# Kernel optimization log

Measured on AMD Instinct MI355X. Metric: run time of the kernel, lower is better.

## Reference

```python
import jax, jax.numpy as jnp
import numpy as np

N = 100000   # nodes
DEG = 16     # in-degree per node
E = N * DEG  # edges
D = 64       # embedding_dim


def mobius_addition(x, y, c):
    xy = jnp.sum(x * y, axis=-1, keepdims=True)
    x2 = jnp.sum(x * x, axis=-1, keepdims=True)
    y2 = jnp.sum(y * y, axis=-1, keepdims=True)
    num = (1 + 2 * c * xy + c * y2) * x + (1 - c * x2) * y
    den = 1 + 2 * c * xy + c * c * x2 * y2
    return num / den


def exp_map(x, v, c):
    vn = jnp.linalg.norm(v, axis=-1, keepdims=True)
    sc = jnp.sqrt(c)
    second = jnp.tanh(sc * vn / 2) * v / (sc * vn)
    return mobius_addition(x, second, c)


def log_map(x, y, c):
    add = mobius_addition(-x, y, c)
    an = jnp.linalg.norm(add, axis=-1, keepdims=True)
    sc = jnp.sqrt(c)
    return 2 / sc * jnp.arctanh(sc * an) * add / an


def setup_inputs() -> dict:
    key = jax.random.key(0)
    ks = jax.random.split(key, 6)
    # scale so points are well inside the Poincare ball (atanh domain)
    x = jax.random.normal(ks[0], (N, D), jnp.float32) * 0.01
    src = jax.random.randint(ks[1], (E,), 0, N, dtype=jnp.int32)
    # every node gets exactly DEG in-edges -> no isolated nodes (avoids 0/0 in exp_map)
    dst = jnp.repeat(jnp.arange(N, dtype=jnp.int32), DEG)
    s = 1.0 / np.sqrt(D)
    Wq = jax.random.normal(ks[2], (D, D), jnp.float32) * s
    Wk = jax.random.normal(ks[3], (D, D), jnp.float32) * s
    Wv = jax.random.normal(ks[4], (D, D), jnp.float32) * s
    bq = jnp.zeros((D,), jnp.float32)
    bk = jnp.zeros((D,), jnp.float32)
    bv = jnp.zeros((D,), jnp.float32)
    curvature = jnp.ones((1,), jnp.float32)
    return {"x": x, "curvature": curvature, "Wq": Wq, "bq": bq, "Wk": Wk,
            "bk": bk, "Wv": Wv, "bv": bv, "src": src, "dst": dst}


def reference(x, curvature, Wq, bq, Wk, bk, Wv, bv, src, dst):
    c = curvature  # (1,), broadcasts against (N,1) keepdim norms
    n = x.shape[0]
    origin = jnp.zeros_like(x[:1])  # (1, D)
    tangent = log_map(origin, x, c)  # (N, D)
    # torch nn.Linear: y = x @ W.T + b
    q = tangent @ Wq.T + bq
    k = tangent @ Wk.T + bk
    v = tangent @ Wv.T + bv
    scale = jnp.asarray(x.shape[-1] ** 0.5, x.dtype)
    # per-edge score: <k[src], q[dst]> / sqrt(d)
    scores = jnp.einsum('ed,ed->e', k[src], q[dst]) / scale  # (E,)
    # segment (per-dst) softmax over incoming edges
    smax = jax.ops.segment_max(scores, dst, num_segments=n)
    ex = jnp.exp(scores - smax[dst])
    ssum = jax.ops.segment_sum(ex, dst, num_segments=n)
    alpha = ex / ssum[dst]  # (E,)
    # weighted scatter-sum of src values
    h = jax.ops.segment_sum(alpha[:, None] * v[src], dst, num_segments=n)  # (N, D)
    return exp_map(origin, h, c)
```

## Files before the change

### kernel.cpp

```cpp
#include <hip/hip_runtime.h>
#include <hip/hip_bf16.h>
#include <math.h>


typedef __attribute__((ext_vector_type(8))) short bf16x8;
typedef __attribute__((ext_vector_type(4))) float f32x4;
typedef __attribute__((ext_vector_type(2))) float f32x2;

static __device__ __forceinline__ short f2bf(float f) {
    union { __hip_bfloat16 h; short s; } u; u.h = __float2bfloat16(f); return u.s;
}
static __device__ __forceinline__ float bflo(unsigned u) {
    return __uint_as_float(u << 16);
}
static __device__ __forceinline__ float bfhi(unsigned u) {
    return __uint_as_float(u & 0xffff0000u);
}

#define TSTRIDE 72
#define SQSTR   72
#define SKSTR   72

__global__ __launch_bounds__(256) void qkv_kernel(
    const float* __restrict__ x,
    const float* __restrict__ cur,
    const float* __restrict__ Wq, const float* __restrict__ bq,
    const float* __restrict__ Wk, const float* __restrict__ bk,
    const float* __restrict__ Wv, const float* __restrict__ bv,
    unsigned short* __restrict__ qb, unsigned char* __restrict__ kf8,
    unsigned short* __restrict__ vb, int N)
{
    __shared__ short tL[128 * TSTRIDE];
    __shared__ short sq[16 * SQSTR];
    __shared__ short sv[16 * SQSTR];
    __shared__ unsigned char sk[16 * SKSTR];
    const int tid = threadIdx.x;
    const int w = tid >> 6, lane = tid & 63;
    const int blockBase = blockIdx.x * 128;
    const float sc = sqrtf(cur[0]);

    const int rr = lane >> 2, p = lane & 3;
    #pragma unroll
    for (int it = 0; it < 2; ++it) {
        const int rloc = w * 32 + it * 16 + rr;
        int row = blockBase + rloc; if (row >= N) row = N - 1;
        const float4* xr = (const float4*)(x + (size_t)row * 64 + p * 16);
        float4 x0 = xr[0], x1 = xr[1], x2 = xr[2], x3 = xr[3];
        float pn = x0.x*x0.x + x0.y*x0.y + x0.z*x0.z + x0.w*x0.w
                 + x1.x*x1.x + x1.y*x1.y + x1.z*x1.z + x1.w*x1.w
                 + x2.x*x2.x + x2.y*x2.y + x2.z*x2.z + x2.w*x2.w
                 + x3.x*x3.x + x3.y*x3.y + x3.z*x3.z + x3.w*x3.w;
        pn += __shfl_xor(pn, 1, 64);
        pn += __shfl_xor(pn, 2, 64);
        float z = sc * sqrtf(pn);
        float ts = (z > 1e-12f) ? (__logf((1.0f + z) / (1.0f - z)) / z) : 2.0f;
        bf16x8 t0, t1;
        t0[0]=f2bf(ts*x0.x); t0[1]=f2bf(ts*x0.y); t0[2]=f2bf(ts*x0.z); t0[3]=f2bf(ts*x0.w);
        t0[4]=f2bf(ts*x1.x); t0[5]=f2bf(ts*x1.y); t0[6]=f2bf(ts*x1.z); t0[7]=f2bf(ts*x1.w);
        t1[0]=f2bf(ts*x2.x); t1[1]=f2bf(ts*x2.y); t1[2]=f2bf(ts*x2.z); t1[3]=f2bf(ts*x2.w);
        t1[4]=f2bf(ts*x3.x); t1[5]=f2bf(ts*x3.y); t1[6]=f2bf(ts*x3.z); t1[7]=f2bf(ts*x3.w);
        bf16x8* dst = (bf16x8*)&tL[rloc * TSTRIDE + p * 16];
        dst[0] = t0; dst[1] = t1;
    }
    __syncthreads();

    const int n16 = lane & 15, quad = lane >> 4;
    bf16x8 Bf[3][2];
    float bias[3];
    int matv[3], col0v[3];
    #pragma unroll
    for (int tt = 0; tt < 3; ++tt) {
        const int tile = w * 3 + tt;
        const int mat = tile >> 2;
        const int col0 = (tile & 3) * 16;
        matv[tt] = mat; col0v[tt] = col0;
        const float* Wm = (mat == 0) ? Wq : (mat == 1) ? Wk : Wv;
        const float* bm = (mat == 0) ? bq : (mat == 1) ? bk : bv;
        const float* srcp = Wm + (col0 + n16) * 64 + quad * 8;
        #pragma unroll
        for (int h = 0; h < 2; ++h) {
            float4 a = *(const float4*)(srcp + h * 32);
            float4 b = *(const float4*)(srcp + h * 32 + 4);
            bf16x8 f;
            f[0]=f2bf(a.x); f[1]=f2bf(a.y); f[2]=f2bf(a.z); f[3]=f2bf(a.w);
            f[4]=f2bf(b.x); f[5]=f2bf(b.y); f[6]=f2bf(b.z); f[7]=f2bf(b.w);
            Bf[tt][h] = f;
        }
        bias[tt] = bm[col0 + n16];
    }

    const int crow = tid >> 4;
    const int c8   = tid & 15;

    for (int nt = 0; nt < 8; ++nt) {
        const short* ar = &tL[(nt * 16 + n16) * TSTRIDE + quad * 8];
        bf16x8 A0 = *(const bf16x8*)ar;
        bf16x8 A1 = *(const bf16x8*)(ar + 32);
        #pragma unroll
        for (int tt = 0; tt < 3; ++tt) {
            f32x4 acc = { bias[tt], bias[tt], bias[tt], bias[tt] };
            acc = __builtin_amdgcn_mfma_f32_16x16x32_bf16(A0, Bf[tt][0], acc, 0, 0, 0);
            acc = __builtin_amdgcn_mfma_f32_16x16x32_bf16(A1, Bf[tt][1], acc, 0, 0, 0);
            const int mat = matv[tt], col0 = col0v[tt];
            #pragma unroll
            for (int r4 = 0; r4 < 4; ++r4) {
                const int rl = quad * 4 + r4;
                const int c  = col0 + n16;
                if (mat == 0) {
                    sq[rl * SQSTR + c] = f2bf(acc[r4]);
                } else if (mat == 1) {
                    int pk = __builtin_amdgcn_cvt_pk_fp8_f32(acc[r4], acc[r4], 0, false);
                    sk[rl * SKSTR + c] = (unsigned char)(pk & 0xff);
                } else {
                    sv[rl * SQSTR + c] = f2bf(acc[r4]);
                }
            }
        }
        __syncthreads();

        const int node = blockBase + nt * 16 + crow;
        if (node < N) {
            *(uint2*)(qb + (size_t)node * 64 + c8 * 4) =
                *(const uint2*)&sq[crow * SQSTR + c8 * 4];
            *(uint2*)(vb + (size_t)node * 64 + c8 * 4) =
                *(const uint2*)&sv[crow * SQSTR + c8 * 4];
            *(unsigned*)(kf8 + (size_t)node * 64 + c8 * 4) =
                *(const unsigned*)&sk[crow * SKSTR + c8 * 4];
        }
        __syncthreads();
    }
}

__global__ __launch_bounds__(256) void attn_kernel(
    const unsigned short* __restrict__ qb, const unsigned char* __restrict__ kf8,
    const unsigned short* __restrict__ vb, const int* __restrict__ src,
    const float* __restrict__ cur,
    float* __restrict__ out, int N)
{
    const int tid = threadIdx.x;
    const int w = tid >> 6, lane = tid & 63;
    int node = blockIdx.x * 4 + w;
    if (node >= N) node = N - 1;

    const int j = lane >> 2, p = lane & 3;
    const int sj = src[node * 16 + j];

    const int half = lane >> 5, l5 = lane & 31;
    const int sbase = 32 * half;
    int srcv[8];
    #pragma unroll
    for (int i = 0; i < 8; ++i) srcv[i] = __shfl(sj, sbase + 4 * i, 64);
    unsigned vraw[8];
    #pragma unroll
    for (int i = 0; i < 8; ++i)
        vraw[i] = *(const unsigned*)(vb + (srcv[i] << 6) + (l5 << 1));

    uint4 kd = *(const uint4*)(kf8 + sj * 64 + p * 16);
    const uint4* qp = (const uint4*)(qb + node * 64 + p * 16);
    uint4 qa = qp[0], qc = qp[1];
    float acc = 0.f;
    {
        f32x2 k0 = __builtin_amdgcn_cvt_pk_f32_fp8(kd.x, false);
        f32x2 k1 = __builtin_amdgcn_cvt_pk_f32_fp8(kd.x, true);
        acc = fmaf(k0[0], bflo(qa.x), acc); acc = fmaf(k0[1], bfhi(qa.x), acc);
        acc = fmaf(k1[0], bflo(qa.y), acc); acc = fmaf(k1[1], bfhi(qa.y), acc);
        k0 = __builtin_amdgcn_cvt_pk_f32_fp8(kd.y, false);
        k1 = __builtin_amdgcn_cvt_pk_f32_fp8(kd.y, true);
        acc = fmaf(k0[0], bflo(qa.z), acc); acc = fmaf(k0[1], bfhi(qa.z), acc);
        acc = fmaf(k1[0], bflo(qa.w), acc); acc = fmaf(k1[1], bfhi(qa.w), acc);
        k0 = __builtin_amdgcn_cvt_pk_f32_fp8(kd.z, false);
        k1 = __builtin_amdgcn_cvt_pk_f32_fp8(kd.z, true);
        acc = fmaf(k0[0], bflo(qc.x), acc); acc = fmaf(k0[1], bfhi(qc.x), acc);
        acc = fmaf(k1[0], bflo(qc.y), acc); acc = fmaf(k1[1], bfhi(qc.y), acc);
        k0 = __builtin_amdgcn_cvt_pk_f32_fp8(kd.w, false);
        k1 = __builtin_amdgcn_cvt_pk_f32_fp8(kd.w, true);
        acc = fmaf(k0[0], bflo(qc.z), acc); acc = fmaf(k0[1], bfhi(qc.z), acc);
        acc = fmaf(k1[0], bflo(qc.w), acc); acc = fmaf(k1[1], bfhi(qc.w), acc);
    }
    acc += __shfl_xor(acc, 1, 64);
    acc += __shfl_xor(acc, 2, 64);
    float score = acc * 0.125f;

    float ex = __expf(score);
    float ssum = ex;
    #pragma unroll
    for (int m = 4; m < 64; m <<= 1) ssum += __shfl_xor(ssum, m, 64);
    float myalpha = ex / ssum;

    float alphav[8];
    #pragma unroll
    for (int i = 0; i < 8; ++i) alphav[i] = __shfl(myalpha, sbase + 4 * i, 64);
    float hx = 0.f, hy = 0.f;
    #pragma unroll
    for (int i = 0; i < 8; ++i) {
        hx = fmaf(alphav[i], bflo(vraw[i]), hx);
        hy = fmaf(alphav[i], bfhi(vraw[i]), hy);
    }
    hx += __shfl_xor(hx, 32, 64);
    hy += __shfl_xor(hy, 32, 64);

    float n2 = hx * hx + hy * hy;
    #pragma unroll
    for (int m = 1; m < 32; m <<= 1) n2 += __shfl_xor(n2, m, 64);
    const float sc = sqrtf(cur[0]);
    float z = sc * sqrtf(n2);
    float e = __expf(z);
    float scale = (z > 1e-12f) ? ((e - 1.0f) / (z * (e + 1.0f))) : 0.5f;
    if (half == 0) {
        float2 o2 = make_float2(scale * hx, scale * hy);
        *(float2*)(out + (size_t)node * 64 + (l5 << 1)) = o2;
    }
}

extern "C" void kernel_launch(void* const* d_in, const int* in_sizes, int n_in,
                              void* d_out, int out_size, void* d_ws, size_t ws_size,
                              hipStream_t stream)
{
    const float* x   = (const float*)d_in[0];
    const float* cur = (const float*)d_in[1];
    const float* Wq  = (const float*)d_in[2];
    const float* bq  = (const float*)d_in[3];
    const float* Wk  = (const float*)d_in[4];
    const float* bk  = (const float*)d_in[5];
    const float* Wv  = (const float*)d_in[6];
    const float* bv  = (const float*)d_in[7];
    const int* src = (const int*)d_in[8];

    const int N = in_sizes[0] / 64;

    unsigned short* qb  = (unsigned short*)d_ws;
    unsigned char*  kf8 = (unsigned char*)(qb + (size_t)N * 64);
    unsigned short* vb  = (unsigned short*)(kf8 + (size_t)N * 64);

    const int blocks1 = (N + 127) / 128;
    const int blocks2 = (N + 3) / 4;
    qkv_kernel<<<blocks1, 256, 0, stream>>>(x, cur, Wq, bq, Wk, bk, Wv, bv,
                                            qb, kf8, vb, N);
    attn_kernel<<<blocks2, 256, 0, stream>>>(qb, kf8, vb, src, cur,
                                             (float*)d_out, N);
}
```

Baseline: 162.6 us.

## Quantize V to per-row int8 and interleave with FP8 K per node

V is now stored as int8 with one fp32 absmax scale per node instead of bf16, and the K (fp8) and V (int8) bytes for each node sit together in a single 128-byte record. This halves the bytes fetched for V in the random src gather and puts each source node's K and V in one contiguous line. The per-row scale is folded into the attention weight before accumulation. The cost is lower V precision and an extra scale gather per edge.

```diff
diff --git a/kernel.cpp b/kernel.cpp
--- a/kernel.cpp
+++ b/kernel.cpp
@@ -20,6 +20,7 @@
 #define TSTRIDE 72
 #define SQSTR   72
 #define SKSTR   72
+#define SVSTR   68
 
 __global__ __launch_bounds__(256) void qkv_kernel(
     const float* __restrict__ x,
@@ -27,13 +28,13 @@
     const float* __restrict__ Wq, const float* __restrict__ bq,
     const float* __restrict__ Wk, const float* __restrict__ bk,
     const float* __restrict__ Wv, const float* __restrict__ bv,
-    unsigned short* __restrict__ qb, unsigned char* __restrict__ kf8,
-    unsigned short* __restrict__ vb, int N)
+    unsigned short* __restrict__ qb, unsigned char* __restrict__ kvl,
+    float* __restrict__ vs, int N)
 {
     __shared__ short tL[128 * TSTRIDE];
     __shared__ short sq[16 * SQSTR];
-    __shared__ short sv[16 * SQSTR];
     __shared__ unsigned char sk[16 * SKSTR];
+    __shared__ float svf[16 * SVSTR];
     const int tid = threadIdx.x;
     const int w = tid >> 6, lane = tid & 63;
     const int blockBase = blockIdx.x * 128;
@@ -112,28 +113,46 @@
                     int pk = __builtin_amdgcn_cvt_pk_fp8_f32(acc[r4], acc[r4], 0, false);
                     sk[rl * SKSTR + c] = (unsigned char)(pk & 0xff);
                 } else {
-                    sv[rl * SQSTR + c] = f2bf(acc[r4]);
+                    svf[rl * SVSTR + c] = acc[r4];
                 }
             }
         }
         __syncthreads();
 
         const int node = blockBase + nt * 16 + crow;
-        if (node < N) {
-            *(uint2*)(qb + (size_t)node * 64 + c8 * 4) =
-                *(const uint2*)&sq[crow * SQSTR + c8 * 4];
-            *(uint2*)(vb + (size_t)node * 64 + c8 * 4) =
-                *(const uint2*)&sv[crow * SQSTR + c8 * 4];
-            *(unsigned*)(kf8 + (size_t)node * 64 + c8 * 4) =
-                *(const unsigned*)&sk[crow * SKSTR + c8 * 4];
+        {
+            f32x4 v4 = *(const f32x4*)&svf[crow * SVSTR + c8 * 4];
+            float m = fmaxf(fmaxf(fabsf(v4[0]), fabsf(v4[1])),
+                            fmaxf(fabsf(v4[2]), fabsf(v4[3])));
+            m = fmaxf(m, __shfl_xor(m, 1, 64));
+            m = fmaxf(m, __shfl_xor(m, 2, 64));
+            m = fmaxf(m, __shfl_xor(m, 4, 64));
+            m = fmaxf(m, __shfl_xor(m, 8, 64));
+            float rm = fmaxf(m, 1e-20f);
+            float inv = 127.0f / rm;
+            float scale = rm * (1.0f / 127.0f);
+            int i0 = __float2int_rn(v4[0] * inv);
+            int i1 = __float2int_rn(v4[1] * inv);
+            int i2 = __float2int_rn(v4[2] * inv);
+            int i3 = __float2int_rn(v4[3] * inv);
+            unsigned pk = (unsigned)(i0 & 255) | ((unsigned)(i1 & 255) << 8)
+                        | ((unsigned)(i2 & 255) << 16) | ((unsigned)(i3 & 255) << 24);
+            if (node < N) {
+                *(uint2*)(qb + (size_t)node * 64 + c8 * 4) =
+                    *(const uint2*)&sq[crow * SQSTR + c8 * 4];
+                *(unsigned*)(kvl + (size_t)node * 128 + c8 * 4) =
+                    *(const unsigned*)&sk[crow * SKSTR + c8 * 4];
+                *(unsigned*)(kvl + (size_t)node * 128 + 64 + c8 * 4) = pk;
+                if (c8 == 0) vs[node] = scale;
+            }
         }
         __syncthreads();
     }
 }
 
 __global__ __launch_bounds__(256) void attn_kernel(
-    const unsigned short* __restrict__ qb, const unsigned char* __restrict__ kf8,
-    const unsigned short* __restrict__ vb, const int* __restrict__ src,
+    const unsigned short* __restrict__ qb, const unsigned char* __restrict__ kvl,
+    const float* __restrict__ vs, const int* __restrict__ src,
     const float* __restrict__ cur,
     float* __restrict__ out, int N)
 {
@@ -150,14 +169,15 @@
     int srcv[8];
     #pragma unroll
     for (int i = 0; i < 8; ++i) srcv[i] = __shfl(sj, sbase + 4 * i, 64);
-    unsigned vraw[8];
+    unsigned short vraw[8];
     #pragma unroll
     for (int i = 0; i < 8; ++i)
-        vraw[i] = *(const unsigned*)(vb + (srcv[i] << 6) + (l5 << 1));
-
-    uint4 kd = *(const uint4*)(kf8 + sj * 64 + p * 16);
-    const uint4* qp = (const uint4*)(qb + node * 64 + p * 16);
+        vraw[i] = *(const unsigned short*)(kvl + (size_t)srcv[i] * 128 + 64 + (l5 << 1));
+
+    uint4 kd = *(const uint4*)(kvl + (size_t)sj * 128 + p * 16);
+    const uint4* qp = (const uint4*)(qb + (size_t)node * 64 + p * 16);
     uint4 qa = qp[0], qc = qp[1];
+    const float sjs = vs[sj];
     float acc = 0.f;
     {
         f32x2 k0 = __builtin_amdgcn_cvt_pk_f32_fp8(kd.x, false);
@@ -185,16 +205,19 @@
     float ssum = ex;
     #pragma unroll
     for (int m = 4; m < 64; m <<= 1) ssum += __shfl_xor(ssum, m, 64);
-    float myalpha = ex / ssum;
-
-    float alphav[8];
-    #pragma unroll
-    for (int i = 0; i < 8; ++i) alphav[i] = __shfl(myalpha, sbase + 4 * i, 64);
+    float myas = (ex / ssum) * sjs;
+
+    float asv[8];
+    #pragma unroll
+    for (int i = 0; i < 8; ++i) asv[i] = __shfl(myas, sbase + 4 * i, 64);
     float hx = 0.f, hy = 0.f;
     #pragma unroll
     for (int i = 0; i < 8; ++i) {
-        hx = fmaf(alphav[i], bflo(vraw[i]), hx);
-        hy = fmaf(alphav[i], bfhi(vraw[i]), hy);
+        int u = (int)vraw[i];
+        float flo = (float)((u << 24) >> 24);
+        float fhi = (float)((short)u >> 8);
+        hx = fmaf(asv[i], flo, hx);
+        hy = fmaf(asv[i], fhi, hy);
     }
     hx += __shfl_xor(hx, 32, 64);
     hy += __shfl_xor(hy, 32, 64);
@@ -229,13 +252,13 @@
     const int N = in_sizes[0] / 64;
 
     unsigned short* qb  = (unsigned short*)d_ws;
-    unsigned char*  kf8 = (unsigned char*)(qb + (size_t)N * 64);
-    unsigned short* vb  = (unsigned short*)(kf8 + (size_t)N * 64);
+    unsigned char*  kvl = (unsigned char*)(qb + (size_t)N * 64);
+    float*          vsc = (float*)(kvl + (size_t)N * 128);
 
     const int blocks1 = (N + 127) / 128;
     const int blocks2 = (N + 3) / 4;
     qkv_kernel<<<blocks1, 256, 0, stream>>>(x, cur, Wq, bq, Wk, bk, Wv, bv,
-                                            qb, kf8, vb, N);
-    attn_kernel<<<blocks2, 256, 0, stream>>>(qb, kf8, vb, src, cur,
+                                            qb, kvl, vsc, N);
+    attn_kernel<<<blocks2, 256, 0, stream>>>(qb, kvl, vsc, src, cur,
                                              (float*)d_out, N);
 }
```

Result: faster. 150.5 us (-7.5%).
